# Optimization experiments

Hardware: AMD Instinct MI355X
Metric: run time of the kernel (lower is better)

Reference implementation:

```python
import jax, jax.numpy as jnp
import numpy as np

B, L, T, H, NL, DFF, DIN = 4096, 64, 256, 8, 4, 1024, 6
HD = T // H
EPS = 1e-9


def setup_inputs() -> dict:
    key = jax.random.key(0)
    ks = jax.random.split(key, 12)
    s = 0.02
    inp = {
        "link_states": jax.random.uniform(ks[0], (B, L, DIN), jnp.float32) * 10.0,
        "link_W1": jax.random.normal(ks[1], (L, DIN, T), jnp.float32) * s,
        "link_b1": jnp.zeros((L, T), jnp.float32),
        "link_W2": jax.random.normal(ks[2], (L, T, T), jnp.float32) * s,
        "link_b2": jnp.zeros((L, T), jnp.float32),
        "Wqkv": jax.random.normal(ks[3], (NL, 3 * T, T), jnp.float32) * s,
        "bqkv": jnp.zeros((NL, 3 * T), jnp.float32),
        "Wo": jax.random.normal(ks[4], (NL, T, T), jnp.float32) * s,
        "bo": jnp.zeros((NL, T), jnp.float32),
        "ln1_g": jnp.ones((NL, T), jnp.float32),
        "ln1_b": jnp.zeros((NL, T), jnp.float32),
        "Wff1": jax.random.normal(ks[5], (NL, DFF, T), jnp.float32) * s,
        "bff1": jnp.zeros((NL, DFF), jnp.float32),
        "Wff2": jax.random.normal(ks[6], (NL, T, DFF), jnp.float32) * s,
        "bff2": jnp.zeros((NL, T), jnp.float32),
        "ln2_g": jnp.ones((NL, T), jnp.float32),
        "ln2_b": jnp.zeros((NL, T), jnp.float32),
        "head_W1": jax.random.normal(ks[7], (T, T), jnp.float32) * s,
        "head_b1": jnp.zeros((T,), jnp.float32),
        "head_W2": jax.random.normal(ks[8], (T, 1), jnp.float32) * s,
        "head_b2": jnp.zeros((1,), jnp.float32),
    }
    return inp


def _layernorm(x, g, b):
    m = x.mean(-1, keepdims=True)
    v = ((x - m) ** 2).mean(-1, keepdims=True)
    return (x - m) * jax.lax.rsqrt(v + 1e-5) * g + b


def _normalize_inputs(x):
    # x: [B, L, 6]
    prop = jnp.clip(x[:, :, 0], 0.0)
    tx = jnp.clip(x[:, :, 1], 0.0)
    sum_pt = prop + tx
    # torch.median returns lower-middle element for even L
    t_ref = jnp.sort(sum_pt, axis=1)[:, (L - 1) // 2][:, None]
    t_ref = jnp.clip(t_ref, 1e-6)
    f0 = prop / t_ref
    f1 = tx / t_ref
    f2 = x[:, :, 2]
    f3 = jnp.log1p(jnp.clip(x[:, :, 3], 0.0))
    f4 = jnp.log1p(jnp.clip(x[:, :, 4], 0.0) / t_ref)
    f5 = jnp.log1p(jnp.clip(x[:, :, 5], 0.0))
    head5 = jnp.stack([f0, f1, f2, f3, f4], axis=-1)  # [B,L,5]
    mean_a = head5.mean(axis=1, keepdims=True)
    std_a = head5.std(axis=1, keepdims=True) + EPS
    head5 = jnp.clip(head5, mean_a - 3.0 * std_a, mean_a + 3.0 * std_a)
    mean = head5.mean(axis=1, keepdims=True)
    std = head5.std(axis=1, keepdims=True) + EPS
    head5 = (head5 - mean) / std
    return jnp.concatenate([head5, f5[:, :, None]], axis=-1)


def _posenc():
    pos = jnp.arange(L, dtype=jnp.float32)[:, None]
    div = jnp.exp(-jnp.log(10000.0) * jnp.arange(0, T, 2, dtype=jnp.float32) / T)
    pe = jnp.zeros((L, T), jnp.float32)
    pe = pe.at[:, 0::2].set(jnp.sin(pos * div))
    pe = pe.at[:, 1::2].set(jnp.cos(pos * div))
    return pe


def _forward(link_states, link_W1, link_b1, link_W2, link_b2, Wqkv, bqkv, Wo, bo,
             ln1_g, ln1_b, Wff1, bff1, Wff2, bff2, ln2_g, ln2_b,
             head_W1, head_b1, head_W2, head_b2):
    x = _normalize_inputs(link_states)  # [B,L,6]
    # per-link (unshared) MLP encoders, batched as grouped matmuls
    h = jax.nn.relu(jnp.einsum('bld,ldt->blt', x, link_W1) + link_b1)
    tok = jnp.einsum('blt,lts->bls', h, link_W2) + link_b2  # [B,L,T]
    y = tok + _posenc()
    scale = 1.0 / np.sqrt(HD)
    for l in range(NL):
        qkv = y @ Wqkv[l].T + bqkv[l]  # [B,L,3T]
        q, k, v = jnp.split(qkv, 3, axis=-1)
        q = q.reshape(B, L, H, HD).transpose(0, 2, 1, 3)
        k = k.reshape(B, L, H, HD).transpose(0, 2, 1, 3)
        v = v.reshape(B, L, H, HD).transpose(0, 2, 1, 3)
        attn = jax.nn.softmax(jnp.einsum('bhqd,bhkd->bhqk', q, k) * scale, axis=-1)
        o = jnp.einsum('bhqk,bhkd->bhqd', attn, v).transpose(0, 2, 1, 3).reshape(B, L, T)
        o = o @ Wo[l].T + bo[l]
        y = _layernorm(y + o, ln1_g[l], ln1_b[l])
        ff = jax.nn.relu(y @ Wff1[l].T + bff1[l]) @ Wff2[l].T + bff2[l]
        y = _layernorm(y + ff, ln2_g[l], ln2_b[l])
    pooled = y.mean(axis=1)  # [B,T]
    hh = jax.nn.relu(pooled @ head_W1 + head_b1)
    values = (hh @ head_W2 + head_b2)[:, 0]  # [B]
    return values


def reference(link_states, link_W1, link_b1, link_W2, link_b2, Wqkv, bqkv, Wo, bo,
              ln1_g, ln1_b, Wff1, bff1, Wff2, bff2, ln2_g, ln2_b,
              head_W1, head_b1, head_W2, head_b2):
    return _forward(link_states, link_W1, link_b1, link_W2, link_b2, Wqkv, bqkv, Wo, bo,
                    ln1_g, ln1_b, Wff1, bff1, Wff2, bff2, ln2_g, ln2_b,
                    head_W1, head_b1, head_W2, head_b2)
```

## Files before the change

### kernel.cpp

```cpp
#include <hip/hip_runtime.h>
#include <cstddef>

#define B_   4096
#define L_   64
#define T_   256
#define H_   8
#define HD_  32
#define NL_  4
#define DFF_ 1024
#define DIN_ 6

typedef unsigned short ushort_t;
typedef __attribute__((ext_vector_type(8))) short bf16x8;
typedef __attribute__((ext_vector_type(4))) float f32x4;

__device__ __forceinline__ float wred_sum(float v) {
#pragma unroll
  for (int off = 32; off >= 1; off >>= 1) v += __shfl_xor(v, off, 64);
  return v;
}
__device__ __forceinline__ ushort_t f2bf(float f) {
  unsigned u = __builtin_bit_cast(unsigned, f);
  u += 0x7fffu + ((u >> 16) & 1u);
  return (ushort_t)(u >> 16);
}
__device__ __forceinline__ float bf2f(ushort_t h) {
  unsigned u = ((unsigned)h) << 16;
  return __builtin_bit_cast(float, u);
}
__device__ __forceinline__ unsigned pk2bf(float a, float b) {
  unsigned r;
  asm volatile("v_cvt_pk_bf16_f32 %0, %1, %2" : "=v"(r) : "v"(a), "v"(b));
  return r;
}
__device__ __forceinline__ void gl16(const ushort_t* g, const ushort_t* l) {
  __builtin_amdgcn_global_load_lds(
      (const __attribute__((address_space(1))) unsigned int*)g,
      (__attribute__((address_space(3))) unsigned int*)l, 16, 0, 0);
}

__global__ __launch_bounds__(256) void normalize_k(const float* __restrict__ xs,
                                                   float* __restrict__ xn) {
  const int w = threadIdx.x >> 6;
  const int b = blockIdx.x * 4 + w;
  const int l = threadIdx.x & 63;
  const float* x = xs + ((size_t)b * L_ + l) * DIN_;
  const float x0 = x[0], x1 = x[1], x2 = x[2], x3 = x[3], x4 = x[4], x5 = x[5];
  const float prop = fmaxf(x0, 0.f), tx = fmaxf(x1, 0.f);
  const float sp = prop + tx;

  __shared__ float sh[4][64];
  __shared__ float med_sh[4];
  sh[w][l] = sp;
  __syncthreads();
  int rk = 0;
#pragma unroll 8
  for (int j = 0; j < 64; ++j) {
    const float vj = sh[w][j];
    rk += (vj < sp) || (vj == sp && j < l);
  }
  if (rk == 31) med_sh[w] = sp;
  __syncthreads();
  const float t_ref = fmaxf(med_sh[w], 1e-6f);

  float f[5];
  f[0] = prop / t_ref;
  f[1] = tx / t_ref;
  f[2] = x2;
  f[3] = log1pf(fmaxf(x3, 0.f));
  f[4] = log1pf(fmaxf(x4, 0.f) / t_ref);
  const float f5 = log1pf(fmaxf(x5, 0.f));

  float* dst = xn + ((size_t)b * L_ + l) * DIN_;
#pragma unroll
  for (int i = 0; i < 5; ++i) {
    float v = f[i];
    float m = wred_sum(v) * (1.f / 64.f);
    float d = v - m;
    float sd = sqrtf(wred_sum(d * d) * (1.f / 64.f)) + 1e-9f;
    const float lo = m - 3.f * sd, hi = m + 3.f * sd;
    const float cv = fminf(fmaxf(v, lo), hi);
    const float m2 = wred_sum(cv) * (1.f / 64.f);
    const float d2 = cv - m2;
    const float sd2 = sqrtf(wred_sum(d2 * d2) * (1.f / 64.f)) + 1e-9f;
    dst[i] = (cv - m2) / sd2;
  }
  dst[5] = f5;
}

__global__ void pe_k(float* __restrict__ pe) {
  const int l = blockIdx.x;
  const int i = threadIdx.x;
  const float div = expf(-9.210340371976184f * (2.0f * i) / 256.0f);
  const float ang = (float)l * div;
  pe[l * T_ + 2 * i]     = sinf(ang);
  pe[l * T_ + 2 * i + 1] = cosf(ang);
}

__global__ void wfrag_k(const float* __restrict__ in, ushort_t* __restrict__ out,
                        int NK, int ksh) {
  const size_t z = blockIdx.z;
  const int idx = blockIdx.x * 256 + threadIdx.x;
  if (idx >= NK) return;
  const int e = idx & 7, li = (idx >> 3) & 15, t = idx >> 7;
  const int ks = t & ((1 << ksh) - 1), cb = t >> ksh;
  const int K = 8 << ksh;
  out[z * (size_t)NK + idx] =
      f2bf(in[z * (size_t)NK + (size_t)(cb * 16 + li) * K + ks * 8 + e]);
}

__global__ void w2t_k(const float* __restrict__ in, ushort_t* __restrict__ out) {
  const int idx = blockIdx.x * 256 + threadIdx.x;
  const int l = idx >> 16, r = idx & 65535, s = r >> 8, t = r & 255;
  out[idx] = f2bf(in[(l << 16) | (t << 8) | s]);
}

__global__ __launch_bounds__(256) void link1_k(const float* __restrict__ xn,
                                               const float* __restrict__ W1,
                                               const float* __restrict__ b1,
                                               ushort_t* __restrict__ h) {
  const size_t r0 = (size_t)blockIdx.x * 16;
  const int col = threadIdx.x;
#pragma unroll
  for (int i = 0; i < 16; ++i) {
    const size_t r = r0 + i;
    const int l = (int)(r & (L_ - 1));
    const float* x = xn + r * DIN_;
    float a = b1[l * T_ + col];
#pragma unroll
    for (int d = 0; d < DIN_; ++d)
      a = fmaf(x[d], W1[((size_t)l * DIN_ + d) * T_ + col], a);
    h[r * T_ + col] = f2bf(fmaxf(a, 0.f));
  }
}

__global__ __launch_bounds__(512) void linkgemm_k(
    const ushort_t* __restrict__ A,
    const ushort_t* __restrict__ W,
    const float* __restrict__ bias,
    const float* __restrict__ pe,
    float* __restrict__ y32) {
  __shared__ ushort_t lA[2][4096];
  __shared__ ushort_t lB[2][8192];
  const int tid = threadIdx.x;
  const int lane = tid & 63, w = tid >> 6;
  const int wr = w >> 2, wc = w & 3;
  const size_t b0 = (size_t)blockIdx.x * 128;
  const int l = blockIdx.z;
  const ushort_t* Az = A + b0 * 16384 + (size_t)l * 256;
  const ushort_t* Wz = W + (size_t)l * 65536;

  const int sm = tid >> 6, sks = (tid >> 4) & 3, srr = tid & 15;

  auto stage = [&](int buf, int kt) {
    gl16(Az + (size_t)(16 * sm + srr) * 16384 + kt + sks * 8,
         &lA[buf][(tid & ~63) * 8]);
#pragma unroll
    for (int rd = 0; rd < 2; ++rd) {
      const int nb = sm + rd * 8;
      gl16(Wz + (size_t)(nb * 16 + srr) * 256 + kt + sks * 8,
           &lB[buf][rd * 4096 + (tid & ~63) * 8]);
    }
  };

  f32x4 acc[4][4];
#pragma unroll
  for (int mi = 0; mi < 4; ++mi)
#pragma unroll
    for (int ni = 0; ni < 4; ++ni) acc[mi][ni] = (f32x4){0.f, 0.f, 0.f, 0.f};

  stage(0, 0);
  asm volatile("s_waitcnt vmcnt(0)" ::: "memory");
  __syncthreads();
  int cur = 0;
  for (int t = 0; t < 8; ++t) {
    if (t + 1 < 8) stage(cur ^ 1, (t + 1) << 5);
    bf16x8 af[4], bfr[4];
#pragma unroll
    for (int mi = 0; mi < 4; ++mi)
      af[mi] = *(const bf16x8*)&lA[cur][((wr * 4 + mi) * 64 + lane) * 8];
#pragma unroll
    for (int ni = 0; ni < 4; ++ni)
      bfr[ni] = *(const bf16x8*)&lB[cur][((wc * 4 + ni) * 64 + lane) * 8];
#pragma unroll
    for (int mi = 0; mi < 4; ++mi)
#pragma unroll
      for (int ni = 0; ni < 4; ++ni)
        acc[mi][ni] = __builtin_amdgcn_mfma_f32_16x16x32_bf16(
            af[mi], bfr[ni], acc[mi][ni], 0, 0, 0);
    asm volatile("s_waitcnt vmcnt(0)" ::: "memory");
    __syncthreads();
    cur ^= 1;
  }

  const int r_in = (lane >> 4) * 4;
  const int c_in = lane & 15;
#pragma unroll
  for (int ni = 0; ni < 4; ++ni) {
    const int cg = wc * 64 + ni * 16 + c_in;
    const float bs = bias[l * 256 + cg] + pe[l * 256 + cg];
#pragma unroll
    for (int mi = 0; mi < 4; ++mi) {
#pragma unroll
      for (int rg = 0; rg < 4; ++rg) {
        const size_t bg = b0 + wr * 64 + mi * 16 + r_in + rg;
        y32[bg * 16384 + l * 256 + cg] = acc[mi][ni][rg] + bs;
      }
    }
  }
}

template <int LAST>
__global__ __launch_bounds__(256, 2) void layer_k(
    float* __restrict__ y32,
    const ushort_t* __restrict__ Wq, const float* __restrict__ bqkv,
    const ushort_t* __restrict__ Wo, const float* __restrict__ bo,
    const float* __restrict__ ln1g, const float* __restrict__ ln1b,
    const ushort_t* __restrict__ Wf1, const float* __restrict__ bf1,
    const ushort_t* __restrict__ Wf2, const float* __restrict__ bf2,
    const float* __restrict__ ln2g, const float* __restrict__ ln2b,
    float* __restrict__ pool) {
  __shared__ ushort_t yF[16384];
  __shared__ ushort_t sc[18432];
  __shared__ float red[4][2][64];
  const int b = blockIdx.x;
  const int tid = threadIdx.x, lane = tid & 63, w = tid >> 6;
  const int li = lane & 15, g = lane >> 4;
  const size_t row0 = (size_t)b * 64;
  const float scale = 0.17677669529663687f;
  ushort_t* bufw = sc + w * 2304;
  ushort_t* vtw  = sc + 9216 + w * 2304;
  ushort_t* zF   = sc;

#pragma unroll
  for (int j = 0; j < 8; ++j) {
    const int u = j * 256 + tid;
    const int row = u & 63, ks = u >> 6;
    const float* src = y32 + (row0 + row) * 256 + ks * 8;
    const float4 a = *(const float4*)src;
    const float4 c = *(const float4*)(src + 4);
    uint4 v;
    v.x = pk2bf(a.x, a.y);
    v.y = pk2bf(a.z, a.w);
    v.z = pk2bf(c.x, c.y);
    v.w = pk2bf(c.z, c.w);
    *(uint4*)&yF[(((row >> 4) * 32 + ks) * 16 + (row & 15)) * 8] = v;
  }
  __syncthreads();

  f32x4 oa2[2][4][2];
#pragma unroll
  for (int hi = 0; hi < 2; ++hi) {
    const int h = w * 2 + hi, hoff = h * 32;

    f32x4 acc[3][2][4];
#pragma unroll
    for (int m = 0; m < 3; ++m)
#pragma unroll
      for (int n = 0; n < 2; ++n)
#pragma unroll
        for (int mi = 0; mi < 4; ++mi) acc[m][n][mi] = (f32x4){0.f, 0.f, 0.f, 0.f};
    __builtin_amdgcn_s_setprio(1);
#pragma unroll
    for (int kt = 0; kt < 8; ++kt) {
      bf16x8 af[4];
#pragma unroll
      for (int mi = 0; mi < 4; ++mi)
        af[mi] = *(const bf16x8*)&yF[((mi * 32 + kt * 4 + g) * 16 + li) * 8];
      bf16x8 bw[3][2];
#pragma unroll
      for (int m = 0; m < 3; ++m)
#pragma unroll
        for (int n = 0; n < 2; ++n)
          bw[m][n] = *(const bf16x8*)(Wq +
              (size_t)(((m * 16 + 2 * h + n) * 32 + kt * 4 + g) * 16 + li) * 8);
#pragma unroll
      for (int m = 0; m < 3; ++m)
#pragma unroll
        for (int n = 0; n < 2; ++n)
#pragma unroll
          for (int mi = 0; mi < 4; ++mi)
            acc[m][n][mi] = __builtin_amdgcn_mfma_f32_16x16x32_bf16(
                af[mi], bw[m][n], acc[m][n][mi], 0, 0, 0);
    }
    __builtin_amdgcn_s_setprio(0);
    float bs[3][2];
#pragma unroll
    for (int m = 0; m < 3; ++m)
#pragma unroll
      for (int n = 0; n < 2; ++n) bs[m][n] = bqkv[m * 256 + hoff + 16 * n + li];

#pragma unroll
    for (int n = 0; n < 2; ++n)
#pragma unroll
      for (int mi = 0; mi < 4; ++mi) {
        const unsigned p0 = pk2bf(acc[0][n][mi][0] + bs[0][n],
                                  acc[0][n][mi][1] + bs[0][n]);
        const unsigned p1 = pk2bf(acc[0][n][mi][2] + bs[0][n],
                                  acc[0][n][mi][3] + bs[0][n]);
        const int base = (16 * mi + 4 * g) * 36 + 16 * n + li;
        bufw[base]       = (ushort_t)p0;
        bufw[base + 36]  = (ushort_t)(p0 >> 16);
        bufw[base + 72]  = (ushort_t)p1;
        bufw[base + 108] = (ushort_t)(p1 >> 16);
      }
    bf16x8 qb[4];
#pragma unroll
    for (int ni = 0; ni < 4; ++ni)
      qb[ni] = *(const bf16x8*)&bufw[(16 * ni + li) * 36 + g * 8];

#pragma unroll
    for (int n = 0; n < 2; ++n)
#pragma unroll
      for (int mi = 0; mi < 4; ++mi) {
        const unsigned p0 = pk2bf(acc[1][n][mi][0] + bs[1][n],
                                  acc[1][n][mi][1] + bs[1][n]);
        const unsigned p1 = pk2bf(acc[1][n][mi][2] + bs[1][n],
                                  acc[1][n][mi][3] + bs[1][n]);
        const int base = (16 * mi + 4 * g) * 36 + 16 * n + li;
        bufw[base]       = (ushort_t)p0;
        bufw[base + 36]  = (ushort_t)(p0 >> 16);
        bufw[base + 72]  = (ushort_t)p1;
        bufw[base + 108] = (ushort_t)(p1 >> 16);
      }
    bf16x8 ka[4];
#pragma unroll
    for (int mi = 0; mi < 4; ++mi)
      ka[mi] = *(const bf16x8*)&bufw[(16 * mi + li) * 36 + g * 8];

#pragma unroll
    for (int n = 0; n < 2; ++n)
#pragma unroll
      for (int mi = 0; mi < 4; ++mi) {
        const unsigned p0 = pk2bf(acc[2][n][mi][0] + bs[2][n],
                                  acc[2][n][mi][1] + bs[2][n]);
        const unsigned p1 = pk2bf(acc[2][n][mi][2] + bs[2][n],
                                  acc[2][n][mi][3] + bs[2][n]);
        *(uint2*)&vtw[(16 * n + li) * 72 + 16 * mi + 4 * g] = make_uint2(p0, p1);
      }
    bf16x8 vb[2][2];
#pragma unroll
    for (int ks = 0; ks < 2; ++ks)
#pragma unroll
      for (int n2 = 0; n2 < 2; ++n2)
        vb[ks][n2] = *(const bf16x8*)&vtw[(16 * n2 + li) * 72 + ks * 32 + g * 8];

#pragma unroll
    for (int mi = 0; mi < 4; ++mi)
#pragma unroll
      for (int n2 = 0; n2 < 2; ++n2) oa2[hi][mi][n2] = (f32x4){0.f, 0.f, 0.f, 0.f};

#pragma unroll
    for (int half = 0; half < 2; ++half) {
      f32x4 s[4][2];
      __builtin_amdgcn_s_setprio(1);
#pragma unroll
      for (int mi = 0; mi < 4; ++mi)
#pragma unroll
        for (int nn = 0; nn < 2; ++nn)
          s[mi][nn] = __builtin_amdgcn_mfma_f32_16x16x32_bf16(
              ka[mi], qb[2 * half + nn], (f32x4){0.f, 0.f, 0.f, 0.f}, 0, 0, 0);
      __builtin_amdgcn_s_setprio(0);

#pragma unroll
      for (int nn = 0; nn < 2; ++nn) {
        float mx = -3.4e38f;
#pragma unroll
        for (int mi = 0; mi < 4; ++mi)
#pragma unroll
          for (int r = 0; r < 4; ++r) {
            s[mi][nn][r] *= scale;
            mx = fmaxf(mx, s[mi][nn][r]);
          }
        mx = fmaxf(mx, __shfl_xor(mx, 16, 64));
        mx = fmaxf(mx, __shfl_xor(mx, 32, 64));
        float sum = 0.f;
#pragma unroll
        for (int mi = 0; mi < 4; ++mi)
#pragma unroll
          for (int r = 0; r < 4; ++r) {
            const float e = expf(s[mi][nn][r] - mx);
            s[mi][nn][r] = e;
            sum += e;
          }
        sum += __shfl_xor(sum, 16, 64);
        sum += __shfl_xor(sum, 32, 64);
        const float inv = 1.f / sum;
        const int qrow = 16 * nn + li;
#pragma unroll
        for (int mi = 0; mi < 4; ++mi) {
          const unsigned lo = pk2bf(s[mi][nn][0] * inv, s[mi][nn][1] * inv);
          const unsigned hi2 = pk2bf(s[mi][nn][2] * inv, s[mi][nn][3] * inv);
          *(uint2*)&bufw[qrow * 72 + 16 * mi + 4 * g] = make_uint2(lo, hi2);
        }
      }

      __builtin_amdgcn_s_setprio(1);
#pragma unroll
      for (int ks = 0; ks < 2; ++ks) {
        bf16x8 pa[2];
#pragma unroll
        for (int m2 = 0; m2 < 2; ++m2)
          pa[m2] = *(const bf16x8*)&bufw[(16 * m2 + li) * 72 + ks * 32 + g * 8];
#pragma unroll
        for (int m2 = 0; m2 < 2; ++m2)
#pragma unroll
          for (int n2 = 0; n2 < 2; ++n2)
            oa2[hi][2 * half + m2][n2] = __builtin_amdgcn_mfma_f32_16x16x32_bf16(
                pa[m2], vb[ks][n2], oa2[hi][2 * half + m2][n2], 0, 0, 0);
      }
      __builtin_amdgcn_s_setprio(0);
    }
  }

  __syncthreads();
#pragma unroll
  for (int hi = 0; hi < 2; ++hi) {
    const int hoff = (2 * w + hi) * 32;
#pragma unroll
    for (int mi = 0; mi < 4; ++mi)
#pragma unroll
      for (int n2 = 0; n2 < 2; ++n2) {
        const unsigned p0 = pk2bf(oa2[hi][mi][n2][0], oa2[hi][mi][n2][1]);
        const unsigned p1 = pk2bf(oa2[hi][mi][n2][2], oa2[hi][mi][n2][3]);
        const int col = hoff + 16 * n2 + li;
        const int base = ((mi * 32 + (col >> 3)) * 16 + 4 * g) * 8 + (col & 7);
        yF[base]      = (ushort_t)p0;
        yF[base + 8]  = (ushort_t)(p0 >> 16);
        yF[base + 16] = (ushort_t)p1;
        yF[base + 24] = (ushort_t)(p1 >> 16);
      }
  }
  __syncthreads();

  f32x4 acc[4][4];
#pragma unroll
  for (int mi = 0; mi < 4; ++mi)
#pragma unroll
    for (int ni = 0; ni < 4; ++ni) acc[mi][ni] = (f32x4){0.f, 0.f, 0.f, 0.f};
  __builtin_amdgcn_s_setprio(1);
#pragma unroll
  for (int kt = 0; kt < 8; ++kt) {
    bf16x8 af[4], bfr[4];
#pragma unroll
    for (int mi = 0; mi < 4; ++mi)
      af[mi] = *(const bf16x8*)&yF[((mi * 32 + kt * 4 + g) * 16 + li) * 8];
#pragma unroll
    for (int ni = 0; ni < 4; ++ni)
      bfr[ni] = *(const bf16x8*)(Wo +
          (size_t)(((4 * w + ni) * 32 + kt * 4 + g) * 16 + li) * 8);
#pragma unroll
    for (int mi = 0; mi < 4; ++mi)
#pragma unroll
      for (int ni = 0; ni < 4; ++ni)
        acc[mi][ni] = __builtin_amdgcn_mfma_f32_16x16x32_bf16(
            af[mi], bfr[ni], acc[mi][ni], 0, 0, 0);
  }
  __builtin_amdgcn_s_setprio(0);

  const int r_in = (lane >> 4) * 4;
  const int c_in = lane & 15;
  float y1r[4][4][4];
#pragma unroll
  for (int mi = 0; mi < 4; ++mi) {
#pragma unroll
    for (int rg = 0; rg < 4; ++rg) {
      const int row_l = 16 * mi + r_in + rg;
      float s1 = 0.f, s2 = 0.f;
#pragma unroll
      for (int ni = 0; ni < 4; ++ni) {
        const int cg = 64 * w + 16 * ni + c_in;
        const float zv = acc[mi][ni][rg] + bo[cg] + y32[(row0 + row_l) * 256 + cg];
        acc[mi][ni][rg] = zv;
        s1 += zv;
        s2 += zv * zv;
      }
#pragma unroll
      for (int off = 1; off <= 8; off <<= 1) {
        s1 += __shfl_xor(s1, off, 64);
        s2 += __shfl_xor(s2, off, 64);
      }
      if (c_in == 0) {
        red[w][0][row_l] = s1;
        red[w][1][row_l] = s2;
      }
    }
  }
  __syncthreads();
#pragma unroll
  for (int mi = 0; mi < 4; ++mi) {
#pragma unroll
    for (int rg = 0; rg < 4; ++rg) {
      const int row_l = 16 * mi + r_in + rg;
      const float S1 = red[0][0][row_l] + red[1][0][row_l] + red[2][0][row_l] + red[3][0][row_l];
      const float S2 = red[0][1][row_l] + red[1][1][row_l] + red[2][1][row_l] + red[3][1][row_l];
      const float m = S1 * (1.f / 256.f);
      const float var = S2 * (1.f / 256.f) - m * m;
      const float rs = rsqrtf(var + 1e-5f);
      float tv[4];
#pragma unroll
      for (int ni = 0; ni < 4; ++ni) {
        const int cg = 64 * w + 16 * ni + c_in;
        tv[ni] = (acc[mi][ni][rg] - m) * rs * ln1g[cg] + ln1b[cg];
        y1r[mi][ni][rg] = tv[ni];
      }
      const unsigned p0 = pk2bf(tv[0], tv[1]);
      const unsigned p1 = pk2bf(tv[2], tv[3]);
#pragma unroll
      for (int ni = 0; ni < 4; ++ni) {
        const int cg = 64 * w + 16 * ni + c_in;
        const unsigned pk = (ni < 2) ? p0 : p1;
        const ushort_t hv = (ni & 1) ? (ushort_t)(pk >> 16) : (ushort_t)pk;
        yF[((mi * 32 + (cg >> 3)) * 16 + (row_l & 15)) * 8 + (cg & 7)] = hv;
      }
    }
  }
  __syncthreads();

  f32x4 acc2[4][4];
#pragma unroll
  for (int mi = 0; mi < 4; ++mi)
#pragma unroll
    for (int ni = 0; ni < 4; ++ni) acc2[mi][ni] = (f32x4){0.f, 0.f, 0.f, 0.f};

#pragma unroll 1
  for (int q = 0; q < 4; ++q) {
#pragma unroll 1
    for (int p = 0; p < 2; ++p) {
      f32x4 acc1[4][2];
#pragma unroll
      for (int mi = 0; mi < 4; ++mi)
#pragma unroll
        for (int n = 0; n < 2; ++n) acc1[mi][n] = (f32x4){0.f, 0.f, 0.f, 0.f};
      __builtin_amdgcn_s_setprio(1);
#pragma unroll
      for (int kt = 0; kt < 8; ++kt) {
        bf16x8 af[4], bw[2];
#pragma unroll
        for (int mi = 0; mi < 4; ++mi)
          af[mi] = *(const bf16x8*)&yF[((mi * 32 + kt * 4 + g) * 16 + li) * 8];
#pragma unroll
        for (int n = 0; n < 2; ++n)
          bw[n] = *(const bf16x8*)(Wf1 +
              (size_t)(((16 * q + 4 * w + 2 * p + n) * 32 + kt * 4 + g) * 16 + li) * 8);
#pragma unroll
        for (int mi = 0; mi < 4; ++mi)
#pragma unroll
          for (int n = 0; n < 2; ++n)
            acc1[mi][n] = __builtin_amdgcn_mfma_f32_16x16x32_bf16(
                af[mi], bw[n], acc1[mi][n], 0, 0, 0);
      }
      __builtin_amdgcn_s_setprio(0);
      if (q && p == 0) __syncthreads();
#pragma unroll
      for (int n = 0; n < 2; ++n) {
        const int kk = 64 * w + 32 * p + 16 * n + li;
        const float bb = bf1[256 * q + kk];
#pragma unroll
        for (int mi = 0; mi < 4; ++mi) {
          const unsigned p0 = pk2bf(fmaxf(acc1[mi][n][0] + bb, 0.f),
                                    fmaxf(acc1[mi][n][1] + bb, 0.f));
          const unsigned p1 = pk2bf(fmaxf(acc1[mi][n][2] + bb, 0.f),
                                    fmaxf(acc1[mi][n][3] + bb, 0.f));
          const int base = ((mi * 32 + (kk >> 3)) * 16 + 4 * g) * 8 + (kk & 7);
          zF[base]      = (ushort_t)p0;
          zF[base + 8]  = (ushort_t)(p0 >> 16);
          zF[base + 16] = (ushort_t)p1;
          zF[base + 24] = (ushort_t)(p1 >> 16);
        }
      }
    }
    __syncthreads();
    __builtin_amdgcn_s_setprio(1);
#pragma unroll
    for (int kt = 0; kt < 8; ++kt) {
      bf16x8 af2[4], bw2[4];
#pragma unroll
      for (int mi = 0; mi < 4; ++mi)
        af2[mi] = *(const bf16x8*)&zF[((mi * 32 + kt * 4 + g) * 16 + li) * 8];
#pragma unroll
      for (int ni = 0; ni < 4; ++ni)
        bw2[ni] = *(const bf16x8*)(Wf2 +
            (size_t)(((4 * w + ni) * 128 + 32 * q + kt * 4 + g) * 16 + li) * 8);
#pragma unroll
      for (int mi = 0; mi < 4; ++mi)
#pragma unroll
        for (int ni = 0; ni < 4; ++ni)
          acc2[mi][ni] = __builtin_amdgcn_mfma_f32_16x16x32_bf16(
              af2[mi], bw2[ni], acc2[mi][ni], 0, 0, 0);
    }
    __builtin_amdgcn_s_setprio(0);
  }

#pragma unroll
  for (int mi = 0; mi < 4; ++mi) {
#pragma unroll
    for (int rg = 0; rg < 4; ++rg) {
      const int row_l = 16 * mi + r_in + rg;
      float s1 = 0.f, s2 = 0.f;
#pragma unroll
      for (int ni = 0; ni < 4; ++ni) {
        const int cg = 64 * w + 16 * ni + c_in;
        const float zv = acc2[mi][ni][rg] + bf2[cg] + y1r[mi][ni][rg];
        acc2[mi][ni][rg] = zv;
        s1 += zv;
        s2 += zv * zv;
      }
#pragma unroll
      for (int off = 1; off <= 8; off <<= 1) {
        s1 += __shfl_xor(s1, off, 64);
        s2 += __shfl_xor(s2, off, 64);
      }
      if (c_in == 0) {
        red[w][0][row_l] = s1;
        red[w][1][row_l] = s2;
      }
    }
  }
  __syncthreads();
  float colsum[4] = {0.f, 0.f, 0.f, 0.f};
#pragma unroll
  for (int mi = 0; mi < 4; ++mi) {
#pragma unroll
    for (int rg = 0; rg < 4; ++rg) {
      const int row_l = 16 * mi + r_in + rg;
      const float S1 = red[0][0][row_l] + red[1][0][row_l] + red[2][0][row_l] + red[3][0][row_l];
      const float S2 = red[0][1][row_l] + red[1][1][row_l] + red[2][1][row_l] + red[3][1][row_l];
      const float m = S1 * (1.f / 256.f);
      const float var = S2 * (1.f / 256.f) - m * m;
      const float rs = rsqrtf(var + 1e-5f);
#pragma unroll
      for (int ni = 0; ni < 4; ++ni) {
        const int cg = 64 * w + 16 * ni + c_in;
        const float v = (acc2[mi][ni][rg] - m) * rs * ln2g[cg] + ln2b[cg];
        if constexpr (LAST) {
          colsum[ni] += v;
        } else {
          y32[(row0 + row_l) * 256 + cg] = v;
        }
      }
    }
  }
  if constexpr (LAST) {
#pragma unroll
    for (int ni = 0; ni < 4; ++ni) {
      float s = colsum[ni];
      s += __shfl_xor(s, 16, 64);
      s += __shfl_xor(s, 32, 64);
      if (g == 0) pool[(size_t)b * 256 + 64 * w + 16 * ni + c_in] = s * (1.f / 64.f);
    }
  }
}

__global__ __launch_bounds__(256) void headgemm_k(
    const float* __restrict__ A, const float* __restrict__ Wt,
    const float* __restrict__ bias, float* __restrict__ out) {
  const int tid = threadIdx.x;
  const int tx = tid & 63, ty = tid >> 6;
  const int cfull = tx * 4;
  const size_t b0 = (size_t)blockIdx.x * 64;

  __shared__ float At[256][68];

  float4 acc[16];
#pragma unroll
  for (int r = 0; r < 16; ++r) acc[r] = make_float4(0.f, 0.f, 0.f, 0.f);
  const int r0 = ty * 16;

  {
    const int rr = tid >> 6;
    const int k4 = (tid & 63) * 4;
#pragma unroll
    for (int p = 0; p < 16; ++p) {
      const int r = p * 4 + rr;
      const float4 v = *(const float4*)(A + (b0 + r) * 256 + k4);
      At[k4 + 0][r] = v.x;
      At[k4 + 1][r] = v.y;
      At[k4 + 2][r] = v.z;
      At[k4 + 3][r] = v.w;
    }
  }
  __syncthreads();
  const float* wp = Wt + cfull;
#pragma unroll 2
  for (int k = 0; k < 256; ++k) {
    const float4 w = *(const float4*)wp;
    wp += 256;
    const float4* ar = (const float4*)(&At[k][r0]);
    const float4 a0 = ar[0], a1 = ar[1], a2 = ar[2], a3 = ar[3];
    const float av[16] = {a0.x, a0.y, a0.z, a0.w, a1.x, a1.y, a1.z, a1.w,
                          a2.x, a2.y, a2.z, a2.w, a3.x, a3.y, a3.z, a3.w};
#pragma unroll
    for (int r = 0; r < 16; ++r) {
      acc[r].x = fmaf(av[r], w.x, acc[r].x);
      acc[r].y = fmaf(av[r], w.y, acc[r].y);
      acc[r].z = fmaf(av[r], w.z, acc[r].z);
      acc[r].w = fmaf(av[r], w.w, acc[r].w);
    }
  }
  const float4 bb = *(const float4*)(bias + cfull);
#pragma unroll
  for (int r = 0; r < 16; ++r) {
    const size_t row = b0 + r0 + r;
    float4 o;
    o.x = fmaxf(acc[r].x + bb.x, 0.f);
    o.y = fmaxf(acc[r].y + bb.y, 0.f);
    o.z = fmaxf(acc[r].z + bb.z, 0.f);
    o.w = fmaxf(acc[r].w + bb.w, 0.f);
    *(float4*)(out + row * 256 + cfull) = o;
  }
}

__global__ __launch_bounds__(64) void head2_k(const float* __restrict__ hh,
                                              const float* __restrict__ W2,
                                              const float* __restrict__ b2,
                                              float* __restrict__ out) {
  const size_t b = blockIdx.x;
  const int lane = threadIdx.x;
  const float4 hv = *(const float4*)(hh + b * T_ + lane * 4);
  const float4 wv = *(const float4*)(W2 + lane * 4);
  float s = hv.x * wv.x + hv.y * wv.y + hv.z * wv.z + hv.w * wv.w;
  s = wred_sum(s);
  if (lane == 0) out[b] = s + b2[0];
}

extern "C" void kernel_launch(void* const* d_in, const int* in_sizes, int n_in,
                              void* d_out, int out_size, void* d_ws, size_t ws_size,
                              hipStream_t stream) {
  const float* link_states = (const float*)d_in[0];
  const float* link_W1 = (const float*)d_in[1];
  const float* link_b1 = (const float*)d_in[2];
  const float* link_W2 = (const float*)d_in[3];
  const float* link_b2 = (const float*)d_in[4];
  const float* Wqkv = (const float*)d_in[5];
  const float* bqkv = (const float*)d_in[6];
  const float* Wo = (const float*)d_in[7];
  const float* bo = (const float*)d_in[8];
  const float* ln1_g = (const float*)d_in[9];
  const float* ln1_b = (const float*)d_in[10];
  const float* Wff1 = (const float*)d_in[11];
  const float* bff1 = (const float*)d_in[12];
  const float* Wff2 = (const float*)d_in[13];
  const float* bff2 = (const float*)d_in[14];
  const float* ln2_g = (const float*)d_in[15];
  const float* ln2_b = (const float*)d_in[16];
  const float* head_W1 = (const float*)d_in[17];
  const float* head_b1 = (const float*)d_in[18];
  const float* head_W2 = (const float*)d_in[19];
  const float* head_b2 = (const float*)d_in[20];

  char* base = (char*)d_ws;
  size_t off = 0;
  auto alloc = [&](size_t bytes) -> char* {
    char* p = base + off;
    off = (off + bytes + 255) & ~(size_t)255;
    return p;
  };

  ushort_t* Wqkv16 = (ushort_t*)alloc((size_t)NL_ * 768 * 256 * 2);
  ushort_t* Wo16   = (ushort_t*)alloc((size_t)NL_ * 256 * 256 * 2);
  ushort_t* Wff116 = (ushort_t*)alloc((size_t)NL_ * 1024 * 256 * 2);
  ushort_t* Wff216 = (ushort_t*)alloc((size_t)NL_ * 256 * 1024 * 2);
  ushort_t* W2T16  = (ushort_t*)alloc((size_t)L_ * 256 * 256 * 2);
  float* pe     = (float*)alloc((size_t)L_ * T_ * 4);
  float* xn     = (float*)alloc((size_t)B_ * L_ * DIN_ * 4);
  float* pooled = (float*)alloc((size_t)B_ * T_ * 4);
  float* hh     = (float*)alloc((size_t)B_ * T_ * 4);

  const size_t fixed_end = off;
  const size_t availB = (ws_size > fixed_end + 65536) ? (ws_size - fixed_end - 65536) : 0;
  int NC = 1;
  while (NC < 32 && (size_t)(B_ / NC) * 98304ull > availB) NC <<= 1;
  const int Bc = B_ / NC;

  float*    y32  = (float*)alloc((size_t)Bc * L_ * T_ * 4);
  ushort_t* hbuf = (ushort_t*)alloc((size_t)Bc * L_ * T_ * 2);

  wfrag_k<<<dim3((768 * 256 + 255) / 256, 1, NL_), 256, 0, stream>>>(
      Wqkv, Wqkv16, 768 * 256, 5);
  wfrag_k<<<dim3((256 * 256 + 255) / 256, 1, NL_), 256, 0, stream>>>(
      Wo, Wo16, 256 * 256, 5);
  wfrag_k<<<dim3((1024 * 256 + 255) / 256, 1, NL_), 256, 0, stream>>>(
      Wff1, Wff116, 1024 * 256, 5);
  wfrag_k<<<dim3((256 * 1024 + 255) / 256, 1, NL_), 256, 0, stream>>>(
      Wff2, Wff216, 256 * 1024, 7);
  w2t_k<<<(L_ * 256 * 256) / 256, 256, 0, stream>>>(link_W2, W2T16);
  pe_k<<<L_, 128, 0, stream>>>(pe);
  normalize_k<<<B_ / 4, 256, 0, stream>>>(link_states, xn);

  for (int c = 0; c < NC; ++c) {
    const size_t bs = (size_t)c * Bc;

    link1_k<<<(Bc * L_) / 16, 256, 0, stream>>>(xn + bs * L_ * DIN_, link_W1,
                                                link_b1, hbuf);
    linkgemm_k<<<dim3(Bc / 128, 1, L_), 512, 0, stream>>>(
        hbuf, W2T16, link_b2, pe, y32);

    for (int l = 0; l < NL_ - 1; ++l) {
      layer_k<0><<<dim3(Bc, 1, 1), 256, 0, stream>>>(
          y32,
          Wqkv16 + (size_t)l * 768 * 256, bqkv + l * 768,
          Wo16 + (size_t)l * 256 * 256, bo + l * 256,
          ln1_g + l * 256, ln1_b + l * 256,
          Wff116 + (size_t)l * 1024 * 256, bff1 + l * 1024,
          Wff216 + (size_t)l * 256 * 1024, bff2 + l * 256,
          ln2_g + l * 256, ln2_b + l * 256, nullptr);
    }
    {
      const int l = NL_ - 1;
      layer_k<1><<<dim3(Bc, 1, 1), 256, 0, stream>>>(
          y32,
          Wqkv16 + (size_t)l * 768 * 256, bqkv + l * 768,
          Wo16 + (size_t)l * 256 * 256, bo + l * 256,
          ln1_g + l * 256, ln1_b + l * 256,
          Wff116 + (size_t)l * 1024 * 256, bff1 + l * 1024,
          Wff216 + (size_t)l * 256 * 1024, bff2 + l * 256,
          ln2_g + l * 256, ln2_b + l * 256, pooled + bs * T_);
    }
  }

  headgemm_k<<<B_ / 64, 256, 0, stream>>>(pooled, head_W1, head_b1, hh);
  head2_k<<<B_, 64, 0, stream>>>(hh, head_W2, head_b2, (float*)d_out);
}
```

Before: 3.543 ms.

## Split layer kernel across eight waves with one attention head per wave

The fused transformer layer kernel now launches 512 threads per block, so each of eight waves handles one attention head. In the output-projection and FFN GEMMs each wave owns 32 output columns instead of 64. The separate V-transpose scratch region is dropped and V is staged through the per-wave buffer before Q and K reuse it, and the LayerNorm row reductions now sum over eight waves. The aim is more resident waves per CU to hide MFMA and memory latency. The cost is a tighter per-thread register budget and more LDS A-fragment reads per MFMA.

Result: slower. 4.022 ms (+13.5%).

```diff
diff --git a/kernel.cpp b/kernel.cpp
--- a/kernel.cpp
+++ b/kernel.cpp
@@ -211,7 +211,7 @@
 }
 
 template <int LAST>
-__global__ __launch_bounds__(256, 2) void layer_k(
+__global__ __launch_bounds__(512, 2) void layer_k(
     float* __restrict__ y32,
     const ushort_t* __restrict__ Wq, const float* __restrict__ bqkv,
     const ushort_t* __restrict__ Wo, const float* __restrict__ bo,
@@ -222,19 +222,21 @@
     float* __restrict__ pool) {
   __shared__ ushort_t yF[16384];
   __shared__ ushort_t sc[18432];
-  __shared__ float red[4][2][64];
+  __shared__ float red[8][2][64];
   const int b = blockIdx.x;
   const int tid = threadIdx.x, lane = tid & 63, w = tid >> 6;
   const int li = lane & 15, g = lane >> 4;
   const size_t row0 = (size_t)b * 64;
   const float scale = 0.17677669529663687f;
   ushort_t* bufw = sc + w * 2304;
-  ushort_t* vtw  = sc + 9216 + w * 2304;
   ushort_t* zF   = sc;
-
-#pragma unroll
-  for (int j = 0; j < 8; ++j) {
-    const int u = j * 256 + tid;
+  const int r_in = g * 4;
+  const int c_in = li;
+  const int hoff = w * 32;
+
+#pragma unroll
+  for (int j = 0; j < 4; ++j) {
+    const int u = j * 512 + tid;
     const int row = u & 63, ks = u >> 6;
     const float* src = y32 + (row0 + row) * 256 + ks * 8;
     const float4 a = *(const float4*)src;
@@ -248,11 +250,12 @@
   }
   __syncthreads();
 
-  f32x4 oa2[2][4][2];
-#pragma unroll
-  for (int hi = 0; hi < 2; ++hi) {
-    const int h = w * 2 + hi, hoff = h * 32;
-
+  f32x4 oa[4][2];
+#pragma unroll
+  for (int mi = 0; mi < 4; ++mi)
+#pragma unroll
+    for (int n2 = 0; n2 < 2; ++n2) oa[mi][n2] = (f32x4){0.f, 0.f, 0.f, 0.f};
+  {
     f32x4 acc[3][2][4];
 #pragma unroll
     for (int m = 0; m < 3; ++m)
@@ -273,7 +276,7 @@
 #pragma unroll
         for (int n = 0; n < 2; ++n)
           bw[m][n] = *(const bf16x8*)(Wq +
-              (size_t)(((m * 16 + 2 * h + n) * 32 + kt * 4 + g) * 16 + li) * 8);
+              (size_t)(((m * 16 + 2 * w + n) * 32 + kt * 4 + g) * 16 + li) * 8);
 #pragma unroll
       for (int m = 0; m < 3; ++m)
 #pragma unroll
@@ -289,6 +292,23 @@
     for (int m = 0; m < 3; ++m)
 #pragma unroll
       for (int n = 0; n < 2; ++n) bs[m][n] = bqkv[m * 256 + hoff + 16 * n + li];
+
+#pragma unroll
+    for (int n = 0; n < 2; ++n)
+#pragma unroll
+      for (int mi = 0; mi < 4; ++mi) {
+        const unsigned p0 = pk2bf(acc[2][n][mi][0] + bs[2][n],
+                                  acc[2][n][mi][1] + bs[2][n]);
+        const unsigned p1 = pk2bf(acc[2][n][mi][2] + bs[2][n],
+                                  acc[2][n][mi][3] + bs[2][n]);
+        *(uint2*)&bufw[(16 * n + li) * 72 + 16 * mi + 4 * g] = make_uint2(p0, p1);
+      }
+    bf16x8 vb[2][2];
+#pragma unroll
+    for (int ks = 0; ks < 2; ++ks)
+#pragma unroll
+      for (int n2 = 0; n2 < 2; ++n2)
+        vb[ks][n2] = *(const bf16x8*)&bufw[(16 * n2 + li) * 72 + ks * 32 + g * 8];
 
 #pragma unroll
     for (int n = 0; n < 2; ++n)
@@ -329,28 +349,6 @@
       ka[mi] = *(const bf16x8*)&bufw[(16 * mi + li) * 36 + g * 8];
 
 #pragma unroll
-    for (int n = 0; n < 2; ++n)
-#pragma unroll
-      for (int mi = 0; mi < 4; ++mi) {
-        const unsigned p0 = pk2bf(acc[2][n][mi][0] + bs[2][n],
-                                  acc[2][n][mi][1] + bs[2][n]);
-        const unsigned p1 = pk2bf(acc[2][n][mi][2] + bs[2][n],
-                                  acc[2][n][mi][3] + bs[2][n]);
-        *(uint2*)&vtw[(16 * n + li) * 72 + 16 * mi + 4 * g] = make_uint2(p0, p1);
-      }
-    bf16x8 vb[2][2];
-#pragma unroll
-    for (int ks = 0; ks < 2; ++ks)
-#pragma unroll
-      for (int n2 = 0; n2 < 2; ++n2)
-        vb[ks][n2] = *(const bf16x8*)&vtw[(16 * n2 + li) * 72 + ks * 32 + g * 8];
-
-#pragma unroll
-    for (int mi = 0; mi < 4; ++mi)
-#pragma unroll
-      for (int n2 = 0; n2 < 2; ++n2) oa2[hi][mi][n2] = (f32x4){0.f, 0.f, 0.f, 0.f};
-
-#pragma unroll
     for (int half = 0; half < 2; ++half) {
       f32x4 s[4][2];
       __builtin_amdgcn_s_setprio(1);
@@ -406,8 +404,8 @@
         for (int m2 = 0; m2 < 2; ++m2)
 #pragma unroll
           for (int n2 = 0; n2 < 2; ++n2)
-            oa2[hi][2 * half + m2][n2] = __builtin_amdgcn_mfma_f32_16x16x32_bf16(
-                pa[m2], vb[ks][n2], oa2[hi][2 * half + m2][n2], 0, 0, 0);
+            oa[2 * half + m2][n2] = __builtin_amdgcn_mfma_f32_16x16x32_bf16(
+                pa[m2], vb[ks][n2], oa[2 * half + m2][n2], 0, 0, 0);
       }
       __builtin_amdgcn_s_setprio(0);
     }
@@ -415,52 +413,46 @@
 
   __syncthreads();
 #pragma unroll
-  for (int hi = 0; hi < 2; ++hi) {
-    const int hoff = (2 * w + hi) * 32;
-#pragma unroll
-    for (int mi = 0; mi < 4; ++mi)
-#pragma unroll
-      for (int n2 = 0; n2 < 2; ++n2) {
-        const unsigned p0 = pk2bf(oa2[hi][mi][n2][0], oa2[hi][mi][n2][1]);
-        const unsigned p1 = pk2bf(oa2[hi][mi][n2][2], oa2[hi][mi][n2][3]);
-        const int col = hoff + 16 * n2 + li;
-        const int base = ((mi * 32 + (col >> 3)) * 16 + 4 * g) * 8 + (col & 7);
-        yF[base]      = (ushort_t)p0;
-        yF[base + 8]  = (ushort_t)(p0 >> 16);
-        yF[base + 16] = (ushort_t)p1;
-        yF[base + 24] = (ushort_t)(p1 >> 16);
-      }
-  }
-  __syncthreads();
-
-  f32x4 acc[4][4];
-#pragma unroll
   for (int mi = 0; mi < 4; ++mi)
 #pragma unroll
-    for (int ni = 0; ni < 4; ++ni) acc[mi][ni] = (f32x4){0.f, 0.f, 0.f, 0.f};
+    for (int n2 = 0; n2 < 2; ++n2) {
+      const unsigned p0 = pk2bf(oa[mi][n2][0], oa[mi][n2][1]);
+      const unsigned p1 = pk2bf(oa[mi][n2][2], oa[mi][n2][3]);
+      const int col = hoff + 16 * n2 + li;
+      const int base = ((mi * 32 + (col >> 3)) * 16 + 4 * g) * 8 + (col & 7);
+      yF[base]      = (ushort_t)p0;
+      yF[base + 8]  = (ushort_t)(p0 >> 16);
+      yF[base + 16] = (ushort_t)p1;
+      yF[base + 24] = (ushort_t)(p1 >> 16);
+    }
+  __syncthreads();
+
+  f32x4 accO[4][2];
+#pragma unroll
+  for (int mi = 0; mi < 4; ++mi)
+#pragma unroll
+    for (int ni = 0; ni < 2; ++ni) accO[mi][ni] = (f32x4){0.f, 0.f, 0.f, 0.f};
   __builtin_amdgcn_s_setprio(1);
 #pragma unroll
   for (int kt = 0; kt < 8; ++kt) {
-    bf16x8 af[4], bfr[4];
+    bf16x8 af[4], bfr[2];
 #pragma unroll
     for (int mi = 0; mi < 4; ++mi)
       af[mi] = *(const bf16x8*)&yF[((mi * 32 + kt * 4 + g) * 16 + li) * 8];
 #pragma unroll
-    for (int ni = 0; ni < 4; ++ni)
+    for (int ni = 0; ni < 2; ++ni)
       bfr[ni] = *(const bf16x8*)(Wo +
-          (size_t)(((4 * w + ni) * 32 + kt * 4 + g) * 16 + li) * 8);
+          (size_t)(((2 * w + ni) * 32 + kt * 4 + g) * 16 + li) * 8);
 #pragma unroll
     for (int mi = 0; mi < 4; ++mi)
 #pragma unroll
-      for (int ni = 0; ni < 4; ++ni)
-        acc[mi][ni] = __builtin_amdgcn_mfma_f32_16x16x32_bf16(
-            af[mi], bfr[ni], acc[mi][ni], 0, 0, 0);
+      for (int ni = 0; ni < 2; ++ni)
+        accO[mi][ni] = __builtin_amdgcn_mfma_f32_16x16x32_bf16(
+            af[mi], bfr[ni], accO[mi][ni], 0, 0, 0);
   }
   __builtin_amdgcn_s_setprio(0);
 
-  const int r_in = (lane >> 4) * 4;
-  const int c_in = lane & 15;
-  float y1r[4][4][4];
+  float y1r[4][2][4];
 #pragma unroll
   for (int mi = 0; mi < 4; ++mi) {
 #pragma unroll
@@ -468,10 +460,10 @@
       const int row_l = 16 * mi + r_in + rg;
       float s1 = 0.f, s2 = 0.f;
 #pragma unroll
-      for (int ni = 0; ni < 4; ++ni) {
-        const int cg = 64 * w + 16 * ni + c_in;
-        const float zv = acc[mi][ni][rg] + bo[cg] + y32[(row0 + row_l) * 256 + cg];
-        acc[mi][ni][rg] = zv;
+      for (int ni = 0; ni < 2; ++ni) {
+        const int cg = 32 * w + 16 * ni + c_in;
+        const float zv = accO[mi][ni][rg] + bo[cg] + y32[(row0 + row_l) * 256 + cg];
+        accO[mi][ni][rg] = zv;
         s1 += zv;
         s2 += zv * zv;
       }
@@ -492,100 +484,99 @@
 #pragma unroll
     for (int rg = 0; rg < 4; ++rg) {
       const int row_l = 16 * mi + r_in + rg;
-      const float S1 = red[0][0][row_l] + red[1][0][row_l] + red[2][0][row_l] + red[3][0][row_l];
-      const float S2 = red[0][1][row_l] + red[1][1][row_l] + red[2][1][row_l] + red[3][1][row_l];
+      float S1 = 0.f, S2 = 0.f;
+#pragma unroll
+      for (int ww = 0; ww < 8; ++ww) {
+        S1 += red[ww][0][row_l];
+        S2 += red[ww][1][row_l];
+      }
       const float m = S1 * (1.f / 256.f);
       const float var = S2 * (1.f / 256.f) - m * m;
       const float rs = rsqrtf(var + 1e-5f);
-      float tv[4];
-#pragma unroll
-      for (int ni = 0; ni < 4; ++ni) {
-        const int cg = 64 * w + 16 * ni + c_in;
-        tv[ni] = (acc[mi][ni][rg] - m) * rs * ln1g[cg] + ln1b[cg];
+      float tv[2];
+#pragma unroll
+      for (int ni = 0; ni < 2; ++ni) {
+        const int cg = 32 * w + 16 * ni + c_in;
+        tv[ni] = (accO[mi][ni][rg] - m) * rs * ln1g[cg] + ln1b[cg];
         y1r[mi][ni][rg] = tv[ni];
       }
       const unsigned p0 = pk2bf(tv[0], tv[1]);
-      const unsigned p1 = pk2bf(tv[2], tv[3]);
-#pragma unroll
-      for (int ni = 0; ni < 4; ++ni) {
-        const int cg = 64 * w + 16 * ni + c_in;
-        const unsigned pk = (ni < 2) ? p0 : p1;
-        const ushort_t hv = (ni & 1) ? (ushort_t)(pk >> 16) : (ushort_t)pk;
+#pragma unroll
+      for (int ni = 0; ni < 2; ++ni) {
+        const int cg = 32 * w + 16 * ni + c_in;
+        const ushort_t hv = ni ? (ushort_t)(p0 >> 16) : (ushort_t)p0;
         yF[((mi * 32 + (cg >> 3)) * 16 + (row_l & 15)) * 8 + (cg & 7)] = hv;
       }
     }
   }
   __syncthreads();
 
-  f32x4 acc2[4][4];
+  f32x4 acc2[4][2];
 #pragma unroll
   for (int mi = 0; mi < 4; ++mi)
 #pragma unroll
-    for (int ni = 0; ni < 4; ++ni) acc2[mi][ni] = (f32x4){0.f, 0.f, 0.f, 0.f};
+    for (int ni = 0; ni < 2; ++ni) acc2[mi][ni] = (f32x4){0.f, 0.f, 0.f, 0.f};
 
 #pragma unroll 1
   for (int q = 0; q < 4; ++q) {
-#pragma unroll 1
-    for (int p = 0; p < 2; ++p) {
-      f32x4 acc1[4][2];
+    f32x4 acc1[4][2];
+#pragma unroll
+    for (int mi = 0; mi < 4; ++mi)
+#pragma unroll
+      for (int n = 0; n < 2; ++n) acc1[mi][n] = (f32x4){0.f, 0.f, 0.f, 0.f};
+    __builtin_amdgcn_s_setprio(1);
+#pragma unroll
+    for (int kt = 0; kt < 8; ++kt) {
+      bf16x8 af[4], bw[2];
 #pragma unroll
       for (int mi = 0; mi < 4; ++mi)
-#pragma unroll
-        for (int n = 0; n < 2; ++n) acc1[mi][n] = (f32x4){0.f, 0.f, 0.f, 0.f};
-      __builtin_amdgcn_s_setprio(1);
-#pragma unroll
-      for (int kt = 0; kt < 8; ++kt) {
-        bf16x8 af[4], bw[2];
-#pragma unroll
-        for (int mi = 0; mi < 4; ++mi)
-          af[mi] = *(const bf16x8*)&yF[((mi * 32 + kt * 4 + g) * 16 + li) * 8];
+        af[mi] = *(const bf16x8*)&yF[((mi * 32 + kt * 4 + g) * 16 + li) * 8];
+#pragma unroll
+      for (int n = 0; n < 2; ++n)
+        bw[n] = *(const bf16x8*)(Wf1 +
+            (size_t)(((16 * q + 2 * w + n) * 32 + kt * 4 + g) * 16 + li) * 8);
+#pragma unroll
+      for (int mi = 0; mi < 4; ++mi)
 #pragma unroll
         for (int n = 0; n < 2; ++n)
-          bw[n] = *(const bf16x8*)(Wf1 +
-              (size_t)(((16 * q + 4 * w + 2 * p + n) * 32 + kt * 4 + g) * 16 + li) * 8);
-#pragma unroll
-        for (int mi = 0; mi < 4; ++mi)
-#pragma unroll
-          for (int n = 0; n < 2; ++n)
-            acc1[mi][n] = __builtin_amdgcn_mfma_f32_16x16x32_bf16(
-                af[mi], bw[n], acc1[mi][n], 0, 0, 0);
-      }
-      __builtin_amdgcn_s_setprio(0);
-      if (q && p == 0) __syncthreads();
-#pragma unroll
-      for (int n = 0; n < 2; ++n) {
-        const int kk = 64 * w + 32 * p + 16 * n + li;
-        const float bb = bf1[256 * q + kk];
-#pragma unroll
-        for (int mi = 0; mi < 4; ++mi) {
-          const unsigned p0 = pk2bf(fmaxf(acc1[mi][n][0] + bb, 0.f),
-                                    fmaxf(acc1[mi][n][1] + bb, 0.f));
-          const unsigned p1 = pk2bf(fmaxf(acc1[mi][n][2] + bb, 0.f),
-                                    fmaxf(acc1[mi][n][3] + bb, 0.f));
-          const int base = ((mi * 32 + (kk >> 3)) * 16 + 4 * g) * 8 + (kk & 7);
-          zF[base]      = (ushort_t)p0;
-          zF[base + 8]  = (ushort_t)(p0 >> 16);
-          zF[base + 16] = (ushort_t)p1;
-          zF[base + 24] = (ushort_t)(p1 >> 16);
-        }
+          acc1[mi][n] = __builtin_amdgcn_mfma_f32_16x16x32_bf16(
+              af[mi], bw[n], acc1[mi][n], 0, 0, 0);
+    }
+    __builtin_amdgcn_s_setprio(0);
+    if (q) __syncthreads();
+#pragma unroll
+    for (int n = 0; n < 2; ++n) {
+      const int kk = 32 * w + 16 * n + li;
+      const float bb = bf1[256 * q + kk];
+#pragma unroll
+      for (int mi = 0; mi < 4; ++mi) {
+        const unsigned p0 = pk2bf(fmaxf(acc1[mi][n][0] + bb, 0.f),
+                                  fmaxf(acc1[mi][n][1] + bb, 0.f));
+        const unsigned p1 = pk2bf(fmaxf(acc1[mi][n][2] + bb, 0.f),
+                                  fmaxf(acc1[mi][n][3] + bb, 0.f));
+        const int base = ((mi * 32 + (kk >> 3)) * 16 + 4 * g) * 8 + (kk & 7);
+        zF[base]      = (ushort_t)p0;
+        zF[base + 8]  = (ushort_t)(p0 >> 16);
+        zF[base + 16] = (ushort_t)p1;
+        zF[base + 24] = (ushort_t)(p1 >> 16);
       }
     }
     __syncthreads();
     __builtin_amdgcn_s_setprio(1);
 #pragma unroll
     for (int kt = 0; kt < 8; ++kt) {
-      bf16x8 af2[4], bw2[4];
+      bf16x8 af2[4], bw2[2];
 #pragma unroll
       for (int mi = 0; mi < 4; ++mi)
         af2[mi] = *(const bf16x8*)&zF[((mi * 32 + kt * 4 + g) * 16 + li) * 8];
 #pragma unroll
-      for (int ni = 0; ni < 4; ++ni)
+      for (int ni = 0; ni < 2; ++ni)
         bw2[ni] = *(const bf16x8*)(Wf2 +
-            (size_t)(((4 * w + ni) * 128 + 32 * q + kt * 4 + g) * 16 + li) * 8);
+            (size_t)(((2 * w + ni) * 128 + 32 * q + kt * 4 + g) * 16 + li) * 8);
 #pragma unroll
       for (int mi = 0; mi < 4; ++mi)
 #pragma unroll
-        for (int ni = 0; ni < 4; ++ni)
+        for (int ni = 0; ni < 2; ++ni)
           acc2[mi][ni] = __builtin_amdgcn_mfma_f32_16x16x32_bf16(
               af2[mi], bw2[ni], acc2[mi][ni], 0, 0, 0);
     }
@@ -599,8 +590,8 @@
       const int row_l = 16 * mi + r_in + rg;
       float s1 = 0.f, s2 = 0.f;
 #pragma unroll
-      for (int ni = 0; ni < 4; ++ni) {
-        const int cg = 64 * w + 16 * ni + c_in;
+      for (int ni = 0; ni < 2; ++ni) {
+        const int cg = 32 * w + 16 * ni + c_in;
         const float zv = acc2[mi][ni][rg] + bf2[cg] + y1r[mi][ni][rg];
         acc2[mi][ni][rg] = zv;
         s1 += zv;
@@ -618,20 +609,24 @@
     }
   }
   __syncthreads();
-  float colsum[4] = {0.f, 0.f, 0.f, 0.f};
+  float colsum[2] = {0.f, 0.f};
 #pragma unroll
   for (int mi = 0; mi < 4; ++mi) {
 #pragma unroll
     for (int rg = 0; rg < 4; ++rg) {
       const int row_l = 16 * mi + r_in + rg;
-      const float S1 = red[0][0][row_l] + red[1][0][row_l] + red[2][0][row_l] + red[3][0][row_l];
-      const float S2 = red[0][1][row_l] + red[1][1][row_l] + red[2][1][row_l] + red[3][1][row_l];
+      float S1 = 0.f, S2 = 0.f;
+#pragma unroll
+      for (int ww = 0; ww < 8; ++ww) {
+        S1 += red[ww][0][row_l];
+        S2 += red[ww][1][row_l];
+      }
       const float m = S1 * (1.f / 256.f);
       const float var = S2 * (1.f / 256.f) - m * m;
       const float rs = rsqrtf(var + 1e-5f);
 #pragma unroll
-      for (int ni = 0; ni < 4; ++ni) {
-        const int cg = 64 * w + 16 * ni + c_in;
+      for (int ni = 0; ni < 2; ++ni) {
+        const int cg = 32 * w + 16 * ni + c_in;
         const float v = (acc2[mi][ni][rg] - m) * rs * ln2g[cg] + ln2b[cg];
         if constexpr (LAST) {
           colsum[ni] += v;
@@ -643,11 +638,11 @@
   }
   if constexpr (LAST) {
 #pragma unroll
-    for (int ni = 0; ni < 4; ++ni) {
+    for (int ni = 0; ni < 2; ++ni) {
       float s = colsum[ni];
       s += __shfl_xor(s, 16, 64);
       s += __shfl_xor(s, 32, 64);
-      if (g == 0) pool[(size_t)b * 256 + 64 * w + 16 * ni + c_in] = s * (1.f / 64.f);
+      if (g == 0) pool[(size_t)b * 256 + 32 * w + 16 * ni + c_in] = s * (1.f / 64.f);
     }
   }
 }
@@ -797,7 +792,7 @@
         hbuf, W2T16, link_b2, pe, y32);
 
     for (int l = 0; l < NL_ - 1; ++l) {
-      layer_k<0><<<dim3(Bc, 1, 1), 256, 0, stream>>>(
+      layer_k<0><<<dim3(Bc, 1, 1), 512, 0, stream>>>(
           y32,
           Wqkv16 + (size_t)l * 768 * 256, bqkv + l * 768,
           Wo16 + (size_t)l * 256 * 256, bo + l * 256,
@@ -808,7 +803,7 @@
     }
     {
       const int l = NL_ - 1;
-      layer_k<1><<<dim3(Bc, 1, 1), 256, 0, stream>>>(
+      layer_k<1><<<dim3(Bc, 1, 1), 512, 0, stream>>>(
           y32,
           Wqkv16 + (size_t)l * 768 * 256, bqkv + l * 768,
           Wo16 + (size_t)l * 256 * 256, bo + l * 256,
```
